# Kernel optimization log

Measured on AMD Instinct MI355X. Metric: run time of the kernel, lower is better.

Reference implementation:

```python
import jax, jax.numpy as jnp
import numpy as np

H_IN = 7
W_IN = 7
SIZE_CHANNEL = 524288


def setup_inputs() -> dict:
    key = jax.random.key(0)
    k1, k2, k3 = jax.random.split(key, 3)
    x = jax.random.normal(k1, (1, SIZE_CHANNEL, H_IN, W_IN), dtype=jnp.float32)
    weight = jax.random.normal(k2, (H_IN * W_IN, SIZE_CHANNEL), dtype=jnp.float32)
    bias = jax.random.normal(k3, (H_IN * W_IN, SIZE_CHANNEL), dtype=jnp.float32)
    return {"x": x, "weight": weight, "bias": bias}


def reference(x, weight, bias):
    # x: (1, C, 7, 7). Replicate swapaxes(1,3) + flatten(end_dim=2) -> (49, C)
    B, C, H, W = x.shape
    xf = jnp.transpose(x, (0, 3, 2, 1)).reshape(B * W * H, C)  # (49, C)
    # Per-channel 7x7 matmul, fully batched over channels:
    Xc = xf.T.reshape(C, H_IN, W_IN)           # (C, 7, 7)
    Wc = weight.T.reshape(C, H_IN, W_IN)       # (C, 7, 7)
    prod = jnp.einsum('cij,cjk->cik', Xc, Wc)  # (C, 7, 7)
    out = prod.reshape(C, H_IN * W_IN).T + bias  # (49, C)
    return out
```

## Files before the change

kernel.cpp:

```cpp
#include <hip/hip_runtime.h>


constexpr int C    = 524288;
constexpr int HW   = 49;
constexpr int BLK  = 128;
constexpr int NF4  = BLK * HW / 4;

__global__ __launch_bounds__(BLK)
void mylinear_kernel(const float* __restrict__ x,
                     const float* __restrict__ w,
                     const float* __restrict__ b,
                     float* __restrict__ out) {
    __shared__ float lds[BLK * HW];

    const int tid   = threadIdx.x;
    const int cbase = blockIdx.x * BLK;

    const float4* __restrict__ xsrc = reinterpret_cast<const float4*>(x + (size_t)cbase * HW);
    float4* ldsv = reinterpret_cast<float4*>(lds);
#pragma unroll
    for (int it = 0; it < (NF4 + BLK - 1) / BLK; ++it) {
        int idx = it * BLK + tid;
        if (idx < NF4) ldsv[idx] = xsrc[idx];
    }
    __syncthreads();

    float xl[HW];
#pragma unroll
    for (int m = 0; m < HW; ++m) xl[m] = lds[tid * HW + m];

    const int c = cbase + tid;

#pragma unroll
    for (int k = 0; k < 7; ++k) {
        float wq[7];
#pragma unroll
        for (int j = 0; j < 7; ++j) wq[j] = w[(size_t)(j * 7 + k) * C + c];
#pragma unroll
        for (int i = 0; i < 7; ++i) {
            const size_t p = (size_t)(i * 7 + k) * C + c;
            float acc = b[p];
#pragma unroll
            for (int j = 0; j < 7; ++j) acc = fmaf(xl[j * 7 + i], wq[j], acc);
            out[p] = acc;
        }
    }
}

extern "C" void kernel_launch(void* const* d_in, const int* in_sizes, int n_in,
                              void* d_out, int out_size, void* d_ws, size_t ws_size,
                              hipStream_t stream) {
    const float* x = (const float*)d_in[0];
    const float* w = (const float*)d_in[1];
    const float* b = (const float*)d_in[2];
    float* out     = (float*)d_out;

    dim3 grid(C / BLK), block(BLK);
    mylinear_kernel<<<grid, block, 0, stream>>>(x, w, b, out);
}
```

Measured before the change: 87.28 us.

## Split output columns across 7 threads per channel with 2D blocks

Each channel is now handled by 7 threads, one per output column k, instead of one thread doing all 49 outputs. Blocks become 64x7 threads covering 64 channels, and each thread reads x directly from LDS instead of keeping all 49 values in registers. This cuts per-thread register pressure and serial work, so more memory requests can be in flight on this bandwidth-bound kernel. In exchange, LDS reads are repeated across the 7 k-threads and the stride-49 LDS accesses may cause bank conflicts.

```diff
diff --git a/kernel.cpp b/kernel.cpp
--- a/kernel.cpp
+++ b/kernel.cpp
@@ -1,49 +1,47 @@
 #include <hip/hip_runtime.h>
 
 
-constexpr int C    = 524288;
-constexpr int HW   = 49;
-constexpr int BLK  = 128;
-constexpr int NF4  = BLK * HW / 4;
+constexpr int C      = 524288;
+constexpr int HW     = 49;
+constexpr int CHB    = 64;
+constexpr int NTHR   = CHB * 7;
+constexpr int NF4    = CHB * HW / 4;
 
-__global__ __launch_bounds__(BLK)
+__global__ __launch_bounds__(NTHR)
 void mylinear_kernel(const float* __restrict__ x,
                      const float* __restrict__ w,
                      const float* __restrict__ b,
                      float* __restrict__ out) {
-    __shared__ float lds[BLK * HW];
+    __shared__ float xs[CHB * HW];
 
-    const int tid   = threadIdx.x;
-    const int cbase = blockIdx.x * BLK;
+    const int tid   = threadIdx.y * CHB + threadIdx.x;
+    const int cbase = blockIdx.x * CHB;
 
     const float4* __restrict__ xsrc = reinterpret_cast<const float4*>(x + (size_t)cbase * HW);
-    float4* ldsv = reinterpret_cast<float4*>(lds);
+    float4* xdst = reinterpret_cast<float4*>(xs);
 #pragma unroll
-    for (int it = 0; it < (NF4 + BLK - 1) / BLK; ++it) {
-        int idx = it * BLK + tid;
-        if (idx < NF4) ldsv[idx] = xsrc[idx];
+    for (int it = 0; it < 2; ++it) {
+        int idx = it * NTHR + tid;
+        if (idx < NF4) xdst[idx] = xsrc[idx];
     }
     __syncthreads();
 
-    float xl[HW];
+    const int l = threadIdx.x;
+    const int k = threadIdx.y;
+    const int c = cbase + l;
+    const float* __restrict__ xl = xs + l * HW;
+
+    float wq[7];
 #pragma unroll
-    for (int m = 0; m < HW; ++m) xl[m] = lds[tid * HW + m];
-
-    const int c = cbase + tid;
+    for (int j = 0; j < 7; ++j) wq[j] = w[(size_t)(j * 7 + k) * C + c];
 
 #pragma unroll
-    for (int k = 0; k < 7; ++k) {
-        float wq[7];
+    for (int i = 0; i < 7; ++i) {
+        const size_t p = (size_t)(i * 7 + k) * C + c;
+        float acc = b[p];
 #pragma unroll
-        for (int j = 0; j < 7; ++j) wq[j] = w[(size_t)(j * 7 + k) * C + c];
-#pragma unroll
-        for (int i = 0; i < 7; ++i) {
-            const size_t p = (size_t)(i * 7 + k) * C + c;
-            float acc = b[p];
-#pragma unroll
-            for (int j = 0; j < 7; ++j) acc = fmaf(xl[j * 7 + i], wq[j], acc);
-            out[p] = acc;
-        }
+        for (int j = 0; j < 7; ++j) acc = fmaf(xl[j * 7 + i], wq[j], acc);
+        out[p] = acc;
     }
 }
 
@@ -55,6 +53,6 @@
     const float* b = (const float*)d_in[2];
     float* out     = (float*)d_out;
 
-    dim3 grid(C / BLK), block(BLK);
+    dim3 grid(C / CHB), block(CHB, 7);
     mylinear_kernel<<<grid, block, 0, stream>>>(x, w, b, out);
 }
```

New measurement: 81.81 us. -6.3%, faster.

## Transpose x into swizzled LDS layout and vectorize weight/bias/output accesses

Applied to the files above, without the earlier changes.

Restructures the kernel so each block handles 256 channels with 7 waves, one per k column. The x tile is staged in LDS transposed to position-major order with an XOR swizzle, so each thread processes 4 channels and does float4 loads of w and bias, float4 LDS reads, and nontemporal float4 stores. The goal is wider global memory transactions and a lower per-thread register load than holding all 49 x values. In exchange, the LDS scatter now needs per-element div/mod index math and 4-byte LDS writes, which may cause bank conflicts.

```diff
diff --git a/kernel.cpp b/kernel.cpp
--- a/kernel.cpp
+++ b/kernel.cpp
@@ -1,49 +1,70 @@
 #include <hip/hip_runtime.h>
 
 
+typedef float f4 __attribute__((ext_vector_type(4)));
+
 constexpr int C    = 524288;
 constexpr int HW   = 49;
-constexpr int BLK  = 128;
-constexpr int NF4  = BLK * HW / 4;
+constexpr int CHB  = 256;
+constexpr int NTHR = 64 * 7;
+constexpr int RS   = CHB;
+constexpr int NF4  = CHB * HW / 4;
 
-__global__ __launch_bounds__(BLK)
+__global__ __launch_bounds__(NTHR)
 void mylinear_kernel(const float* __restrict__ x,
                      const float* __restrict__ w,
                      const float* __restrict__ b,
                      float* __restrict__ out) {
-    __shared__ float lds[BLK * HW];
+    __shared__ float xs[HW * CHB];
 
-    const int tid   = threadIdx.x;
-    const int cbase = blockIdx.x * BLK;
+    const int tid   = threadIdx.y * 64 + threadIdx.x;
+    const int cbase = blockIdx.x * CHB;
 
-    const float4* __restrict__ xsrc = reinterpret_cast<const float4*>(x + (size_t)cbase * HW);
-    float4* ldsv = reinterpret_cast<float4*>(lds);
+    const f4* __restrict__ xsrc = reinterpret_cast<const f4*>(x + (size_t)cbase * HW);
 #pragma unroll
-    for (int it = 0; it < (NF4 + BLK - 1) / BLK; ++it) {
-        int idx = it * BLK + tid;
-        if (idx < NF4) ldsv[idx] = xsrc[idx];
+    for (int it = 0; it < NF4 / NTHR; ++it) {
+        const int idx = it * NTHR + tid;
+        const f4 v = xsrc[idx];
+#pragma unroll
+        for (int t = 0; t < 4; ++t) {
+            const int e   = idx * 4 + t;
+            const int cl  = e / HW;
+            const int pos = e % HW;
+            const int g   = (pos >> 2) & 7;
+            const int sl  = (cl >> 2) ^ g;
+            xs[pos * RS + (sl << 2 | (cl & 3))] = v[t];
+        }
     }
     __syncthreads();
 
-    float xl[HW];
+    const int q  = threadIdx.x;
+    const int kk = threadIdx.y;
+    const int c  = cbase + (q << 2);
+
+    f4 wq[7];
 #pragma unroll
-    for (int m = 0; m < HW; ++m) xl[m] = lds[tid * HW + m];
-
-    const int c = cbase + tid;
+    for (int j = 0; j < 7; ++j)
+        wq[j] = *reinterpret_cast<const f4*>(w + (size_t)(j * 7 + kk) * C + c);
 
 #pragma unroll
-    for (int k = 0; k < 7; ++k) {
-        float wq[7];
+    for (int i = 0; i < 7; ++i) {
+        f4 xv[7];
 #pragma unroll
-        for (int j = 0; j < 7; ++j) wq[j] = w[(size_t)(j * 7 + k) * C + c];
+        for (int j = 0; j < 7; ++j) {
+            const int pos = j * 7 + i;
+            const int g   = (pos >> 2) & 7;
+            xv[j] = *reinterpret_cast<const f4*>(xs + pos * RS + ((q ^ g) << 2));
+        }
+        const size_t p = (size_t)(i * 7 + kk) * C + c;
+        f4 acc = *reinterpret_cast<const f4*>(b + p);
 #pragma unroll
-        for (int i = 0; i < 7; ++i) {
-            const size_t p = (size_t)(i * 7 + k) * C + c;
-            float acc = b[p];
-#pragma unroll
-            for (int j = 0; j < 7; ++j) acc = fmaf(xl[j * 7 + i], wq[j], acc);
-            out[p] = acc;
+        for (int j = 0; j < 7; ++j) {
+            acc.x = fmaf(xv[j].x, wq[j].x, acc.x);
+            acc.y = fmaf(xv[j].y, wq[j].y, acc.y);
+            acc.z = fmaf(xv[j].z, wq[j].z, acc.z);
+            acc.w = fmaf(xv[j].w, wq[j].w, acc.w);
         }
+        __builtin_nontemporal_store(acc, reinterpret_cast<f4*>(out + p));
     }
 }
 
@@ -55,6 +76,6 @@
     const float* b = (const float*)d_in[2];
     float* out     = (float*)d_out;
 
-    dim3 grid(C / BLK), block(BLK);
+    dim3 grid(C / CHB), block(64, 7);
     mylinear_kernel<<<grid, block, 0, stream>>>(x, w, b, out);
 }
```

Result: faster. 73.24 us (-16.1%).
